# Performance work log

Measured on AMD Instinct MI355X. Metric: run time of the kernel, lower is better.

## Reference

```python
import math
import jax, jax.numpy as jnp
import numpy as np

B, N, D = 4, 4096, 1024
H, M = 16, 64
HD = D // H  # 64
EPS = 1e-6


def favor_features(data, proj):
    # data: [B,H,N,hd], proj: [M,hd] -> [B,H,N,M]
    hd = data.shape[-1]
    m = proj.shape[0]
    dn = data / math.sqrt(hd)
    norm_sq = 0.5 * jnp.sum(dn * dn, axis=-1, keepdims=True)  # [B,H,N,1]
    comb = jnp.einsum('bhnd,md->bhnm', dn, proj) - norm_sq
    comb = comb - jnp.max(comb, axis=-1, keepdims=True)
    return jnp.exp(comb) / math.sqrt(m) + EPS


def setup_inputs() -> dict:
    key = jax.random.key(0)
    ks = jax.random.split(key, 6)
    x = jax.random.normal(ks[0], (B, N, D), dtype=jnp.float32)
    qkv_w = jax.random.normal(ks[1], (3 * D, D), dtype=jnp.float32) * (1.0 / math.sqrt(D))
    qkv_b = jnp.zeros((3 * D,), dtype=jnp.float32)
    proj_w = jax.random.normal(ks[2], (D, D), dtype=jnp.float32) * (1.0 / math.sqrt(D))
    proj_b = jnp.zeros((D,), dtype=jnp.float32)
    pm = jax.random.normal(ks[3], (M, HD), dtype=jnp.float32)
    pm = pm / jnp.linalg.norm(pm, axis=-1, keepdims=True)
    return {"x": x, "qkv_w": qkv_w, "qkv_b": qkv_b, "proj_w": proj_w,
            "proj_b": proj_b, "projection_matrix": pm}


def reference(x, qkv_w, qkv_b, proj_w, proj_b, projection_matrix):
    b, n, d = x.shape
    qkv = x @ qkv_w.T + qkv_b                      # [B,N,3D]
    qkv = qkv.reshape(b, n, 3, H, HD)
    qkv = jnp.transpose(qkv, (2, 0, 3, 1, 4))      # [3,B,H,N,hd]
    q, k, v = qkv[0], qkv[1], qkv[2]
    q_p = favor_features(q, projection_matrix)     # [B,H,N,M]
    k_p = favor_features(k, projection_matrix)     # [B,H,N,M]
    kv = jnp.einsum('bhnm,bhnv->bhmv', k_p, v)     # [B,H,M,hd]
    out = jnp.einsum('bhnm,bhmv->bhnv', q_p, kv)   # [B,H,N,hd]
    k_sum = jnp.sum(k_p, axis=2)                   # [B,H,M]
    normalizer = jnp.einsum('bhnm,bhm->bhn', q_p, k_sum)[..., None]
    out = out / (normalizer + EPS)
    out = jnp.transpose(out, (0, 2, 1, 3)).reshape(b, n, d)
    return out @ proj_w.T + proj_b
```

## Files before the change

### kernel.cpp

```cpp
#include <hip/hip_runtime.h>
#include <math.h>

#define B_  4
#define N_  4096
#define D_  1024
#define H_  16
#define HD_ 64
#define M_  64
#define TD_ 3072
#define EPS_ 1e-6f

typedef __attribute__((ext_vector_type(8))) short short8;
typedef __attribute__((ext_vector_type(4))) float floatx4;
typedef unsigned int uint32;
typedef unsigned short ushort;

__device__ __forceinline__ void cvt2(float f0, float f1, uint32& hp, uint32& lp)
{
    uint32 b0 = __float_as_uint(f0), b1 = __float_as_uint(f1);
    hp = (b1 & 0xFFFF0000u) | (b0 >> 16);
    float l0 = f0 - __uint_as_float(b0 & 0xFFFF0000u);
    float l1 = f1 - __uint_as_float(b1 & 0xFFFF0000u);
    lp = (__float_as_uint(l1) & 0xFFFF0000u) | (__float_as_uint(l0) >> 16);
}

__global__ __launch_bounds__(256) void split_kernel(
    const float* __restrict__ src, ushort* __restrict__ hi,
    ushort* __restrict__ lo, int n)
{
    size_t i = ((size_t)blockIdx.x * 256 + threadIdx.x) * 8;
    if (i >= (size_t)n) return;
    float4 f0 = *(const float4*)(src + i);
    float4 f1 = *(const float4*)(src + i + 4);
    uint4 h, l;
    cvt2(f0.x, f0.y, h.x, l.x); cvt2(f0.z, f0.w, h.y, l.y);
    cvt2(f1.x, f1.y, h.z, l.z); cvt2(f1.z, f1.w, h.w, l.w);
    *(uint4*)(hi + i) = h;
    *(uint4*)(lo + i) = l;
}

#define LDSTR 40

__global__ __launch_bounds__(256, 2) void gemm_presplit_nt_bias(
    const ushort* __restrict__ Ah, const ushort* __restrict__ Al,
    const ushort* __restrict__ Bh, const ushort* __restrict__ Bl,
    const float* __restrict__ bias, float* __restrict__ C,
    int Nx, int Kx)
{
    __shared__ __align__(16) ushort AhiS[128*LDSTR], AloS[128*LDSTR];
    __shared__ __align__(16) ushort BhiS[128*LDSTR], BloS[128*LDSTR];

    const int t    = threadIdx.x;
    const int bm   = blockIdx.y * 128, bn = blockIdx.x * 128;
    const int lane = t & 63, wave = t >> 6;
    const int wm   = wave >> 1, wn = wave & 1;
    const int l16  = lane & 15, quad = lane >> 4;
    const int r    = t >> 1;
    const int ko   = (t & 1) * 16;

    floatx4 acc[4][4];
#pragma unroll
    for (int i = 0; i < 4; i++)
#pragma unroll
        for (int j = 0; j < 4; j++) acc[i][j] = (floatx4)0.f;

    const ushort* aph = Ah + (size_t)(bm + r) * Kx + ko;
    const ushort* apl = Al + (size_t)(bm + r) * Kx + ko;
    const ushort* bph = Bh + (size_t)(bn + r) * Kx + ko;
    const ushort* bpl = Bl + (size_t)(bn + r) * Kx + ko;

    for (int k0 = 0; k0 < Kx; k0 += 32) {
        uint4 vah0 = *(const uint4*)(aph + k0);
        uint4 vah1 = *(const uint4*)(aph + k0 + 8);
        uint4 val0 = *(const uint4*)(apl + k0);
        uint4 val1 = *(const uint4*)(apl + k0 + 8);
        uint4 vbh0 = *(const uint4*)(bph + k0);
        uint4 vbh1 = *(const uint4*)(bph + k0 + 8);
        uint4 vbl0 = *(const uint4*)(bpl + k0);
        uint4 vbl1 = *(const uint4*)(bpl + k0 + 8);

        __syncthreads();

        *(uint4*)&AhiS[r*LDSTR + ko]     = vah0;
        *(uint4*)&AhiS[r*LDSTR + ko + 8] = vah1;
        *(uint4*)&AloS[r*LDSTR + ko]     = val0;
        *(uint4*)&AloS[r*LDSTR + ko + 8] = val1;
        *(uint4*)&BhiS[r*LDSTR + ko]     = vbh0;
        *(uint4*)&BhiS[r*LDSTR + ko + 8] = vbh1;
        *(uint4*)&BloS[r*LDSTR + ko]     = vbl0;
        *(uint4*)&BloS[r*LDSTR + ko + 8] = vbl1;

        __syncthreads();

        short8 ah[4], al[4], bh[4], bl[4];
#pragma unroll
        for (int mi = 0; mi < 4; mi++) {
            int row = (wm*64 + mi*16 + l16) * LDSTR + quad*8;
            ah[mi] = *(const short8*)&AhiS[row];
            al[mi] = *(const short8*)&AloS[row];
        }
#pragma unroll
        for (int ni = 0; ni < 4; ni++) {
            int row = (wn*64 + ni*16 + l16) * LDSTR + quad*8;
            bh[ni] = *(const short8*)&BhiS[row];
            bl[ni] = *(const short8*)&BloS[row];
        }
#pragma unroll
        for (int mi = 0; mi < 4; mi++)
#pragma unroll
            for (int ni = 0; ni < 4; ni++) {
                floatx4 d = acc[mi][ni];
                d = __builtin_amdgcn_mfma_f32_16x16x32_bf16(ah[mi], bh[ni], d, 0, 0, 0);
                d = __builtin_amdgcn_mfma_f32_16x16x32_bf16(al[mi], bh[ni], d, 0, 0, 0);
                d = __builtin_amdgcn_mfma_f32_16x16x32_bf16(ah[mi], bl[ni], d, 0, 0, 0);
                acc[mi][ni] = d;
            }
    }

    float bia[4];
#pragma unroll
    for (int ni = 0; ni < 4; ni++)
        bia[ni] = bias[bn + wn*64 + ni*16 + l16];
#pragma unroll
    for (int mi = 0; mi < 4; mi++)
#pragma unroll
        for (int rr = 0; rr < 4; rr++) {
            int row = bm + wm*64 + mi*16 + quad*4 + rr;
            float* crow = C + (size_t)row * Nx + bn + wn*64 + l16;
#pragma unroll
            for (int ni = 0; ni < 4; ni++)
                crow[ni*16] = acc[mi][ni][rr] + bia[ni];
        }
}

__device__ __forceinline__ void gload16(const void* g, void* l)
{
    __builtin_amdgcn_global_load_lds(
        (const __attribute__((address_space(1))) unsigned int*)g,
        (__attribute__((address_space(3))) unsigned int*)l,
        16, 0, 0);
}

#define BAR()  asm volatile("s_barrier" ::: "memory")

__global__ __launch_bounds__(512, 2) void gemm256_pipe(
    const ushort* __restrict__ Ah, const ushort* __restrict__ Al,
    const ushort* __restrict__ Bh, const ushort* __restrict__ Bl,
    const float* __restrict__ bias, float* __restrict__ C,
    int Nx, int Kx)
{
    __shared__ __align__(16) ushort lds[65536];

    const int t    = threadIdx.x;
    const int wave = t >> 6, lane = t & 63;
    const int wm   = wave >> 2, wn = wave & 3;
    const int l16  = lane & 15, quad = lane >> 4;

    const int gx  = gridDim.x;
    const int nwg = gx * gridDim.y;
    int bid = blockIdx.y * gx + blockIdx.x;
    const int cpx = nwg >> 3;
    bid = (bid & 7) * cpx + (bid >> 3);
    const int bm = (bid / gx) * 256;
    const int bn = (bid % gx) * 256;

    const int r0   = t >> 2;
    const int cswz = ((((t & 3) << 4) ^ ((t & 0x18) << 1)) >> 1);
    const size_t aOff = (size_t)(bm + r0) * Kx + cswz;
    const size_t bOff = (size_t)(bn + r0) * Kx + cswz;

    const int ucol = (quad * 8) ^ ((l16 & 6) << 2);
    const int aRB  = (wm * 64 + l16) * 32 + ucol;
    const int bRB  = (wn * 32 + l16) * 32 + ucol;

    floatx4 acc[8][4];
#pragma unroll
    for (int i = 0; i < 8; i++)
#pragma unroll
        for (int j = 0; j < 4; j++) acc[i][j] = (floatx4)0.f;

#define STAGE_A2(NB, KT) do {                                                 \
    size_t g0_ = (size_t)(KT) * 32;                                           \
    gload16(Ah + aOff + g0_,                   &lds[(NB) + wave*512]);        \
    gload16(Al + aOff + g0_,                   &lds[(NB) + 8192 + wave*512]); \
    gload16(Ah + aOff + (size_t)128*Kx + g0_,  &lds[(NB) + 4096 + wave*512]); \
    gload16(Al + aOff + (size_t)128*Kx + g0_,  &lds[(NB) + 12288 + wave*512]);\
} while (0)
#define STAGE_B2(NB, KT) do {                                                 \
    size_t g0_ = (size_t)(KT) * 32;                                           \
    gload16(Bh + bOff + g0_,                   &lds[(NB) + 16384 + wave*512]);\
    gload16(Bl + bOff + g0_,                   &lds[(NB) + 24576 + wave*512]);\
    gload16(Bh + bOff + (size_t)128*Kx + g0_,  &lds[(NB) + 20480 + wave*512]);\
    gload16(Bl + bOff + (size_t)128*Kx + g0_,  &lds[(NB) + 28672 + wave*512]);\
} while (0)

    const int NT = Kx >> 5;

    STAGE_A2(0, 0);
    STAGE_B2(0, 0);
    asm volatile("s_waitcnt vmcnt(0)" ::: "memory");
    BAR();

    for (int kt = 0; kt < NT; kt++) {
        const int cb  = (kt & 1) << 15;
        const int nb  = cb ^ 32768;
        const int ktn = (kt + 1 < NT) ? kt + 1 : NT - 1;

        short8 ah_[4], al_[4], bh_[4], bl_[4];
        const int aB0 = cb + aRB;
        const int bB0 = cb + 16384 + bRB;

        STAGE_A2(nb, ktn);
        STAGE_B2(nb, ktn);

#pragma unroll
        for (int g = 0; g < 4; g++) {
            bh_[g] = *(const short8*)&lds[bB0 + (g >> 1)*4096 + (g & 1)*512];
            bl_[g] = *(const short8*)&lds[bB0 + 8192 + (g >> 1)*4096 + (g & 1)*512];
        }
#pragma unroll
        for (int mi = 0; mi < 4; mi++) {
            ah_[mi] = *(const short8*)&lds[aB0 + mi*512];
            al_[mi] = *(const short8*)&lds[aB0 + 8192 + mi*512];
        }
        __builtin_amdgcn_s_setprio(1);
#pragma unroll
        for (int mi = 0; mi < 4; mi++)
#pragma unroll
            for (int g = 0; g < 4; g++) {
                floatx4 d = acc[mi][g];
                d = __builtin_amdgcn_mfma_f32_16x16x32_bf16(ah_[mi], bh_[g], d, 0, 0, 0);
                d = __builtin_amdgcn_mfma_f32_16x16x32_bf16(al_[mi], bh_[g], d, 0, 0, 0);
                d = __builtin_amdgcn_mfma_f32_16x16x32_bf16(ah_[mi], bl_[g], d, 0, 0, 0);
                acc[mi][g] = d;
            }
        __builtin_amdgcn_s_setprio(0);

#pragma unroll
        for (int mi = 0; mi < 4; mi++) {
            ah_[mi] = *(const short8*)&lds[aB0 + 4096 + mi*512];
            al_[mi] = *(const short8*)&lds[aB0 + 12288 + mi*512];
        }
        __builtin_amdgcn_s_setprio(1);
#pragma unroll
        for (int mi = 0; mi < 4; mi++)
#pragma unroll
            for (int g = 0; g < 4; g++) {
                floatx4 d = acc[4 + mi][g];
                d = __builtin_amdgcn_mfma_f32_16x16x32_bf16(ah_[mi], bh_[g], d, 0, 0, 0);
                d = __builtin_amdgcn_mfma_f32_16x16x32_bf16(al_[mi], bh_[g], d, 0, 0, 0);
                d = __builtin_amdgcn_mfma_f32_16x16x32_bf16(ah_[mi], bl_[g], d, 0, 0, 0);
                acc[4 + mi][g] = d;
            }
        __builtin_amdgcn_s_setprio(0);

        asm volatile("s_waitcnt vmcnt(0)" ::: "memory");
        BAR();
    }

#pragma unroll
    for (int f = 0; f < 8; f++) {
        const int row = bm + (f >> 2)*128 + wm*64 + (f & 3)*16 + quad*4;
#pragma unroll
        for (int g = 0; g < 4; g++) {
            const int col = bn + (g >> 1)*128 + wn*32 + (g & 1)*16 + l16;
            const float bb = bias[col];
#pragma unroll
            for (int rr = 0; rr < 4; rr++)
                C[(size_t)(row + rr) * Nx + col] = acc[f][g][rr] + bb;
        }
    }
#undef STAGE_A2
#undef STAGE_B2
}

__global__ __launch_bounds__(256) void favor_features_kernel(
    const float* __restrict__ qkvb, const float* __restrict__ proj,
    float* __restrict__ qp, float* __restrict__ kp)
{
    __shared__ float  projT[64*64];
    __shared__ float4 dnbuf[4][64];
    const int t = threadIdx.x;
    const int wave = t >> 6, lane = t & 63;
    const int part = blockIdx.y;
    float* outp = (part == 0) ? qp : kp;

    for (int i = t; i < 4096; i += 256)
        projT[(i & 63) * 64 + (i >> 6)] = proj[i];
    __syncthreads();

    const int h = blockIdx.x >> 6;
    const int n0 = (blockIdx.x & 63) * 64;
    const float* src = qkvb + part * D_ + h * HD_ + lane;

    for (int iter = 0; iter < 4; iter++) {
        const int n = n0 + iter * 16 + wave * 4;
        float v0 = src[(size_t)(n+0) * TD_];
        float v1 = src[(size_t)(n+1) * TD_];
        float v2 = src[(size_t)(n+2) * TD_];
        float v3 = src[(size_t)(n+3) * TD_];
        float4 dn = make_float4(v0*0.125f, v1*0.125f, v2*0.125f, v3*0.125f);
        dnbuf[wave][lane] = dn;
        float s0 = dn.x*dn.x, s1 = dn.y*dn.y, s2 = dn.z*dn.z, s3 = dn.w*dn.w;
#pragma unroll
        for (int off = 32; off >= 1; off >>= 1) {
            s0 += __shfl_xor(s0, off, 64);
            s1 += __shfl_xor(s1, off, 64);
            s2 += __shfl_xor(s2, off, 64);
            s3 += __shfl_xor(s3, off, 64);
        }
        float c0 = -0.5f*s0, c1 = -0.5f*s1, c2 = -0.5f*s2, c3 = -0.5f*s3;
#pragma unroll
        for (int d = 0; d < 64; d++) {
            float p = projT[d*64 + lane];
            float4 q = dnbuf[wave][d];
            c0 = fmaf(q.x, p, c0);
            c1 = fmaf(q.y, p, c1);
            c2 = fmaf(q.z, p, c2);
            c3 = fmaf(q.w, p, c3);
        }
        float m0 = c0, m1 = c1, m2 = c2, m3 = c3;
#pragma unroll
        for (int off = 32; off >= 1; off >>= 1) {
            m0 = fmaxf(m0, __shfl_xor(m0, off, 64));
            m1 = fmaxf(m1, __shfl_xor(m1, off, 64));
            m2 = fmaxf(m2, __shfl_xor(m2, off, 64));
            m3 = fmaxf(m3, __shfl_xor(m3, off, 64));
        }
        float r0 = expf(c0 - m0) * 0.125f + EPS_;
        float r1 = expf(c1 - m1) * 0.125f + EPS_;
        float r2 = expf(c2 - m2) * 0.125f + EPS_;
        float r3 = expf(c3 - m3) * 0.125f + EPS_;
        size_t orow = ((size_t)h * N_ + n) * 64 + lane;
        outp[orow]       = r0;
        outp[orow + 64]  = r1;
        outp[orow + 128] = r2;
        outp[orow + 192] = r3;
    }
}

__global__ __launch_bounds__(256) void kv_partial_kernel(
    const float* __restrict__ qkvb, const float* __restrict__ kp,
    float* __restrict__ kvpart, float* __restrict__ kspart)
{
    const int t = threadIdx.x;
    const int h = blockIdx.x;
    const int c = blockIdx.y;
    const int n0 = c * 128;
    const int m0 = (t & 15) * 4;
    const int v0 = (t >> 4) * 4;

    const float* kpsrc = kp + ((size_t)h * N_ + n0) * 64 + m0;
    const float* vsrc  = qkvb + (size_t)n0 * TD_ + 2 * D_ + h * HD_ + v0;

    float acc[4][4];
#pragma unroll
    for (int i = 0; i < 4; i++)
#pragma unroll
        for (int j = 0; j < 4; j++) acc[i][j] = 0.f;
    float ks[4] = {0.f, 0.f, 0.f, 0.f};

#pragma unroll 4
    for (int n = 0; n < 128; n++) {
        float4 kq = *(const float4*)(kpsrc + (size_t)n * 64);
        float4 vq = *(const float4*)(vsrc  + (size_t)n * TD_);
        acc[0][0] = fmaf(kq.x, vq.x, acc[0][0]);
        acc[0][1] = fmaf(kq.x, vq.y, acc[0][1]);
        acc[0][2] = fmaf(kq.x, vq.z, acc[0][2]);
        acc[0][3] = fmaf(kq.x, vq.w, acc[0][3]);
        acc[1][0] = fmaf(kq.y, vq.x, acc[1][0]);
        acc[1][1] = fmaf(kq.y, vq.y, acc[1][1]);
        acc[1][2] = fmaf(kq.y, vq.z, acc[1][2]);
        acc[1][3] = fmaf(kq.y, vq.w, acc[1][3]);
        acc[2][0] = fmaf(kq.z, vq.x, acc[2][0]);
        acc[2][1] = fmaf(kq.z, vq.y, acc[2][1]);
        acc[2][2] = fmaf(kq.z, vq.z, acc[2][2]);
        acc[2][3] = fmaf(kq.z, vq.w, acc[2][3]);
        acc[3][0] = fmaf(kq.w, vq.x, acc[3][0]);
        acc[3][1] = fmaf(kq.w, vq.y, acc[3][1]);
        acc[3][2] = fmaf(kq.w, vq.z, acc[3][2]);
        acc[3][3] = fmaf(kq.w, vq.w, acc[3][3]);
        if (v0 == 0) {
            ks[0] += kq.x; ks[1] += kq.y; ks[2] += kq.z; ks[3] += kq.w;
        }
    }

    float* kvp = kvpart + (((size_t)h * 32 + c) * 4096) + m0 * 64 + v0;
#pragma unroll
    for (int i = 0; i < 4; i++)
        *(float4*)(kvp + i * 64) = make_float4(acc[i][0], acc[i][1], acc[i][2], acc[i][3]);

    if (v0 == 0) {
        float* ksp = kspart + ((size_t)h * 32 + c) * 64 + m0;
        *(float4*)ksp = make_float4(ks[0], ks[1], ks[2], ks[3]);
    }
}

__global__ __launch_bounds__(256) void kv_reduce_kernel(
    const float* __restrict__ kvpart, const float* __restrict__ kspart,
    float* __restrict__ kv, float* __restrict__ ksum)
{
    const int t = threadIdx.x;
    const int h = blockIdx.x;
    const int e0 = (blockIdx.y * 256 + t) * 4;

    float4 s = make_float4(0.f, 0.f, 0.f, 0.f);
    float kss = 0.f;
    const bool doks = (blockIdx.y == 0) && (t < 64);

    for (int c = 0; c < 32; c++) {
        float4 x = *(const float4*)(kvpart + (((size_t)h * 32 + c) * 4096) + e0);
        s.x += x.x; s.y += x.y; s.z += x.z; s.w += x.w;
        if (doks) kss += kspart[((size_t)h * 32 + c) * 64 + t];
    }

    *(float4*)(kv + (size_t)h * 4096 + e0) = s;
    if (doks) ksum[h * 64 + t] = kss;
}

__global__ __launch_bounds__(256) void out_kernel(
    const float* __restrict__ qp, const float* __restrict__ kv,
    const float* __restrict__ ksum, ushort* __restrict__ attn_hi,
    ushort* __restrict__ attn_lo)
{
    __shared__ float  kvs[4096];
    __shared__ float  kss[64];
    __shared__ float4 qbuf[4][64];
    const int t = threadIdx.x, lane = t & 63, wave = t >> 6;
    const int h = blockIdx.x;
    const int n0 = blockIdx.y * 64;

    for (int i = t; i < 4096; i += 256) kvs[i] = kv[(size_t)h * 4096 + i];
    if (t < 64) kss[t] = ksum[h * 64 + t];
    __syncthreads();

    const float* qsrc = qp + (size_t)h * N_ * 64 + lane;
    const size_t dbase = h * HD_ + lane;

    for (int iter = 0; iter < 4; iter++) {
        const int n = n0 + iter * 16 + wave * 4;
        float q0 = qsrc[(size_t)(n+0) * 64];
        float q1 = qsrc[(size_t)(n+1) * 64];
        float q2 = qsrc[(size_t)(n+2) * 64];
        float q3 = qsrc[(size_t)(n+3) * 64];
        qbuf[wave][lane] = make_float4(q0, q1, q2, q3);
        float t0 = q0 * kss[lane], t1 = q1 * kss[lane];
        float t2 = q2 * kss[lane], t3 = q3 * kss[lane];
#pragma unroll
        for (int off = 32; off >= 1; off >>= 1) {
            t0 += __shfl_xor(t0, off, 64);
            t1 += __shfl_xor(t1, off, 64);
            t2 += __shfl_xor(t2, off, 64);
            t3 += __shfl_xor(t3, off, 64);
        }
        float a0 = 0.f, a1 = 0.f, a2 = 0.f, a3 = 0.f;
#pragma unroll
        for (int m = 0; m < 64; m++) {
            float kvv = kvs[m*64 + lane];
            float4 q = qbuf[wave][m];
            a0 = fmaf(q.x, kvv, a0);
            a1 = fmaf(q.y, kvv, a1);
            a2 = fmaf(q.z, kvv, a2);
            a3 = fmaf(q.w, kvv, a3);
        }
        float r[4];
        r[0] = a0 / (t0 + EPS_); r[1] = a1 / (t1 + EPS_);
        r[2] = a2 / (t2 + EPS_); r[3] = a3 / (t3 + EPS_);
#pragma unroll
        for (int i = 0; i < 4; i++) {
            uint32 bits = __float_as_uint(r[i]);
            float lof = r[i] - __uint_as_float(bits & 0xFFFF0000u);
            size_t idx = (size_t)(n + i) * D_ + dbase;
            attn_hi[idx] = (ushort)(bits >> 16);
            attn_lo[idx] = (ushort)(__float_as_uint(lof) >> 16);
        }
    }
}

extern "C" void kernel_launch(void* const* d_in, const int* in_sizes, int n_in,
                              void* d_out, int out_size, void* d_ws, size_t ws_size,
                              hipStream_t stream)
{
    const float* x      = (const float*)d_in[0];
    const float* qkv_w  = (const float*)d_in[1];
    const float* qkv_b  = (const float*)d_in[2];
    const float* proj_w = (const float*)d_in[3];
    const float* proj_b = (const float*)d_in[4];
    const float* pm     = (const float*)d_in[5];
    float* out = (float*)d_out;
    float* ws  = (float*)d_ws;

    const bool tierA = ws_size >= 327553024ULL;
    const bool tierB = ws_size >= 176558080ULL;

    if (tierA) {
        float* qkvbA  = ws;
        float* qp     = qkvbA + 50331648;
        float* kp     = qp + 4194304;
        float* kvb    = kp + 4194304;
        float* ksum   = kvb + 65536;
        float* kvpart = ksum + 1024;
        float* kspart = kvpart + 2097152;
        float* axw    = kspart + 32768;
        float* wsplit = axw + 16777216;

        ushort* xw_hi    = (ushort*)axw;
        ushort* xw_lo    = xw_hi + 16777216;
        ushort* attn_hi  = xw_hi;
        ushort* attn_lo  = xw_lo;
        ushort* qkvw_hi  = (ushort*)wsplit;
        ushort* qkvw_lo  = qkvw_hi + 3145728;
        ushort* projw_hi = qkvw_lo + 3145728;
        ushort* projw_lo = projw_hi + 1048576;

        split_kernel<<<1536, 256, 0, stream>>>(qkv_w, qkvw_hi, qkvw_lo, TD_*D_);
        split_kernel<<<512,  256, 0, stream>>>(proj_w, projw_hi, projw_lo, D_*D_);
        split_kernel<<<8192, 256, 0, stream>>>(x, xw_hi, xw_lo, B_*N_*D_);

        gemm256_pipe<<<dim3(12, 64), 512, 0, stream>>>(
            xw_hi, xw_lo, qkvw_hi, qkvw_lo, qkv_b, qkvbA, TD_, D_);

        for (int b = 0; b < B_; b++) {
            const float* qkvb = qkvbA + (size_t)b * N_ * TD_;
            dim3 g2(1024, 2);
            favor_features_kernel<<<g2, 256, 0, stream>>>(qkvb, pm, qp, kp);
            dim3 g3(16, 32);
            kv_partial_kernel<<<g3, 256, 0, stream>>>(qkvb, kp, kvpart, kspart);
            kv_reduce_kernel<<<dim3(16, 4), 256, 0, stream>>>(kvpart, kspart, kvb, ksum);
            dim3 g4(16, 64);
            out_kernel<<<g4, 256, 0, stream>>>(qp, kvb, ksum,
                attn_hi + (size_t)b * N_ * D_, attn_lo + (size_t)b * N_ * D_);
        }

        gemm256_pipe<<<dim3(4, 64), 512, 0, stream>>>(
            attn_hi, attn_lo, projw_hi, projw_lo, proj_b, out, D_, D_);
    } else if (tierB) {
        float* qkvb   = ws;
        float* qp     = ws + 12582912;
        float* kp     = qp + 4194304;
        float* kvb    = kp + 4194304;
        float* ksum   = kvb + 65536;
        float* kvpart = ksum + 1024;
        float* kspart = kvpart + 2097152;
        float* wsplit = kspart + 32768;
        float* attnA  = wsplit + 4194304;

        ushort* xw_hi    = (ushort*)qp;
        ushort* xw_lo    = xw_hi + 4194304;
        ushort* qkvw_hi  = (ushort*)wsplit;
        ushort* qkvw_lo  = qkvw_hi + 3145728;
        ushort* projw_hi = qkvw_lo + 3145728;
        ushort* projw_lo = projw_hi + 1048576;
        ushort* attnA_hi = (ushort*)attnA;
        ushort* attnA_lo = attnA_hi + 16777216;

        split_kernel<<<1536, 256, 0, stream>>>(qkv_w, qkvw_hi, qkvw_lo, TD_*D_);
        split_kernel<<<512,  256, 0, stream>>>(proj_w, projw_hi, projw_lo, D_*D_);

        for (int b = 0; b < B_; b++) {
            const float* xb = x + (size_t)b * N_ * D_;
            split_kernel<<<2048, 256, 0, stream>>>(xb, xw_hi, xw_lo, N_*D_);
            gemm256_pipe<<<dim3(12, 16), 512, 0, stream>>>(
                xw_hi, xw_lo, qkvw_hi, qkvw_lo, qkv_b, qkvb, TD_, D_);
            dim3 g2(1024, 2);
            favor_features_kernel<<<g2, 256, 0, stream>>>(qkvb, pm, qp, kp);
            dim3 g3(16, 32);
            kv_partial_kernel<<<g3, 256, 0, stream>>>(qkvb, kp, kvpart, kspart);
            kv_reduce_kernel<<<dim3(16, 4), 256, 0, stream>>>(kvpart, kspart, kvb, ksum);
            dim3 g4(16, 64);
            out_kernel<<<g4, 256, 0, stream>>>(qp, kvb, ksum,
                attnA_hi + (size_t)b * N_ * D_, attnA_lo + (size_t)b * N_ * D_);
        }

        gemm256_pipe<<<dim3(4, 64), 512, 0, stream>>>(
            attnA_hi, attnA_lo, projw_hi, projw_lo, proj_b, out, D_, D_);
    } else {
        float* qkvb   = ws;
        float* qpreg  = ws + 12582912;
        float* kpreg  = qpreg + 4194304;
        float* kvb    = kpreg + 4194304;
        float* ksum   = kvb + 65536;
        float* kvpart = ksum + 1024;
        float* kspart = kvpart + 2097152;
        float* wsplit = kspart + 32768;

        ushort* xw_hi   = (ushort*)qpreg;
        ushort* xw_lo   = xw_hi + 4194304;
        float*  qp      = qpreg;
        float*  kp      = kpreg;
        ushort* attn_hi = (ushort*)kpreg;
        ushort* attn_lo = attn_hi + 4194304;
        ushort* qkvw_hi = (ushort*)wsplit;
        ushort* qkvw_lo = qkvw_hi + 3145728;
        ushort* projw_hi= qkvw_lo + 3145728;
        ushort* projw_lo= projw_hi + 1048576;

        split_kernel<<<TD_*D_/2048, 256, 0, stream>>>(qkv_w, qkvw_hi, qkvw_lo, TD_*D_);
        split_kernel<<<D_*D_/2048,  256, 0, stream>>>(proj_w, projw_hi, projw_lo, D_*D_);

        for (int b = 0; b < B_; b++) {
            const float* xb = x + (size_t)b * N_ * D_;
            float* outb = out + (size_t)b * N_ * D_;

            split_kernel<<<N_*D_/2048, 256, 0, stream>>>(xb, xw_hi, xw_lo, N_*D_);

            gemm256_pipe<<<dim3(12, 16), 512, 0, stream>>>(
                xw_hi, xw_lo, qkvw_hi, qkvw_lo, qkv_b, qkvb, TD_, D_);

            dim3 g2(1024, 2);
            favor_features_kernel<<<g2, 256, 0, stream>>>(qkvb, pm, qp, kp);

            dim3 g3(16, 32);
            kv_partial_kernel<<<g3, 256, 0, stream>>>(qkvb, kp, kvpart, kspart);
            kv_reduce_kernel<<<dim3(16, 4), 256, 0, stream>>>(kvpart, kspart, kvb, ksum);

            dim3 g4(16, 64);
            out_kernel<<<g4, 256, 0, stream>>>(qp, kvb, ksum, attn_hi, attn_lo);

            dim3 g5(D_ / 128, N_ / 128);
            gemm_presplit_nt_bias<<<g5, 256, 0, stream>>>(
                attn_hi, attn_lo, projw_hi, projw_lo, proj_b, outb, D_, D_);
        }
    }
}
```

Before: 949.1 us.

## Fuse FAVOR feature map with KV accumulation via atomics and reschedule GEMM staging

Merges the q/k feature-map kernel, the KV partial kernel and the KV reduce kernel into one kernel. K features are kept in shared memory instead of being written to global, and per-chunk partials are reduced with float atomicAdd into a buffer zeroed by a new small kernel. Separately, the pipelined GEMM now issues the B-tile staging after the first MFMA half, with explicit lgkmcnt waits and scheduling barriers, to spread global loads across the compute. Atomics make the KV summation order nondeterministic, and the fused kernel uses more LDS per block.

```diff
diff --git a/kernel.cpp b/kernel.cpp
--- a/kernel.cpp
+++ b/kernel.cpp
@@ -39,6 +39,12 @@
     *(uint4*)(lo + i) = l;
 }
 
+__global__ __launch_bounds__(256) void zero_kernel(float* __restrict__ p)
+{
+    int i = (blockIdx.x * 256 + threadIdx.x) * 4;
+    if (i < 66560) *(float4*)(p + i) = make_float4(0.f, 0.f, 0.f, 0.f);
+}
+
 #define LDSTR 40
 
 __global__ __launch_bounds__(256, 2) void gemm_presplit_nt_bias(
@@ -142,6 +148,7 @@
 }
 
 #define BAR()  asm volatile("s_barrier" ::: "memory")
+#define SBAR() __builtin_amdgcn_sched_barrier(0)
 
 __global__ __launch_bounds__(512, 2) void gemm256_pipe(
     const ushort* __restrict__ Ah, const ushort* __restrict__ Al,
@@ -211,7 +218,6 @@
         const int bB0 = cb + 16384 + bRB;
 
         STAGE_A2(nb, ktn);
-        STAGE_B2(nb, ktn);
 
 #pragma unroll
         for (int g = 0; g < 4; g++) {
@@ -223,6 +229,8 @@
             ah_[mi] = *(const short8*)&lds[aB0 + mi*512];
             al_[mi] = *(const short8*)&lds[aB0 + 8192 + mi*512];
         }
+        asm volatile("s_waitcnt lgkmcnt(0)" ::: "memory");
+        SBAR();
         __builtin_amdgcn_s_setprio(1);
 #pragma unroll
         for (int mi = 0; mi < 4; mi++)
@@ -235,12 +243,16 @@
                 acc[mi][g] = d;
             }
         __builtin_amdgcn_s_setprio(0);
-
+        SBAR();
+
+        STAGE_B2(nb, ktn);
 #pragma unroll
         for (int mi = 0; mi < 4; mi++) {
             ah_[mi] = *(const short8*)&lds[aB0 + 4096 + mi*512];
             al_[mi] = *(const short8*)&lds[aB0 + 12288 + mi*512];
         }
+        asm volatile("s_waitcnt lgkmcnt(0)" ::: "memory");
+        SBAR();
         __builtin_amdgcn_s_setprio(1);
 #pragma unroll
         for (int mi = 0; mi < 4; mi++)
@@ -253,6 +265,7 @@
                 acc[4 + mi][g] = d;
             }
         __builtin_amdgcn_s_setprio(0);
+        SBAR();
 
         asm volatile("s_waitcnt vmcnt(0)" ::: "memory");
         BAR();
@@ -274,84 +287,87 @@
 #undef STAGE_B2
 }
 
-__global__ __launch_bounds__(256) void favor_features_kernel(
+__global__ __launch_bounds__(256) void favor_kv_kernel(
     const float* __restrict__ qkvb, const float* __restrict__ proj,
-    float* __restrict__ qp, float* __restrict__ kp)
+    float* __restrict__ qp, float* __restrict__ kvb, float* __restrict__ ksum)
 {
     __shared__ float  projT[64*64];
+    __shared__ float  kpL[128*64];
     __shared__ float4 dnbuf[4][64];
-    const int t = threadIdx.x;
-    const int wave = t >> 6, lane = t & 63;
-    const int part = blockIdx.y;
-    float* outp = (part == 0) ? qp : kp;
+    const int t = threadIdx.x, wave = t >> 6, lane = t & 63;
+    const int h  = blockIdx.x;
+    const int n0 = blockIdx.y * 128;
 
     for (int i = t; i < 4096; i += 256)
         projT[(i & 63) * 64 + (i >> 6)] = proj[i];
     __syncthreads();
 
-    const int h = blockIdx.x >> 6;
-    const int n0 = (blockIdx.x & 63) * 64;
-    const float* src = qkvb + part * D_ + h * HD_ + lane;
-
-    for (int iter = 0; iter < 4; iter++) {
-        const int n = n0 + iter * 16 + wave * 4;
-        float v0 = src[(size_t)(n+0) * TD_];
-        float v1 = src[(size_t)(n+1) * TD_];
-        float v2 = src[(size_t)(n+2) * TD_];
-        float v3 = src[(size_t)(n+3) * TD_];
-        float4 dn = make_float4(v0*0.125f, v1*0.125f, v2*0.125f, v3*0.125f);
-        dnbuf[wave][lane] = dn;
-        float s0 = dn.x*dn.x, s1 = dn.y*dn.y, s2 = dn.z*dn.z, s3 = dn.w*dn.w;
-#pragma unroll
-        for (int off = 32; off >= 1; off >>= 1) {
-            s0 += __shfl_xor(s0, off, 64);
-            s1 += __shfl_xor(s1, off, 64);
-            s2 += __shfl_xor(s2, off, 64);
-            s3 += __shfl_xor(s3, off, 64);
-        }
-        float c0 = -0.5f*s0, c1 = -0.5f*s1, c2 = -0.5f*s2, c3 = -0.5f*s3;
-#pragma unroll
-        for (int d = 0; d < 64; d++) {
-            float p = projT[d*64 + lane];
-            float4 q = dnbuf[wave][d];
-            c0 = fmaf(q.x, p, c0);
-            c1 = fmaf(q.y, p, c1);
-            c2 = fmaf(q.z, p, c2);
-            c3 = fmaf(q.w, p, c3);
-        }
-        float m0 = c0, m1 = c1, m2 = c2, m3 = c3;
-#pragma unroll
-        for (int off = 32; off >= 1; off >>= 1) {
-            m0 = fmaxf(m0, __shfl_xor(m0, off, 64));
-            m1 = fmaxf(m1, __shfl_xor(m1, off, 64));
-            m2 = fmaxf(m2, __shfl_xor(m2, off, 64));
-            m3 = fmaxf(m3, __shfl_xor(m3, off, 64));
-        }
-        float r0 = expf(c0 - m0) * 0.125f + EPS_;
-        float r1 = expf(c1 - m1) * 0.125f + EPS_;
-        float r2 = expf(c2 - m2) * 0.125f + EPS_;
-        float r3 = expf(c3 - m3) * 0.125f + EPS_;
+#define FAVOR_ROWS(PART, EMIT)                                                \
+    {                                                                         \
+        const float* src = qkvb + (PART) * D_ + h * HD_ + lane;               \
+        for (int iter = 0; iter < 8; iter++) {                                \
+            const int n = n0 + iter * 16 + wave * 4;                          \
+            float v0 = src[(size_t)(n+0) * TD_];                              \
+            float v1 = src[(size_t)(n+1) * TD_];                              \
+            float v2 = src[(size_t)(n+2) * TD_];                              \
+            float v3 = src[(size_t)(n+3) * TD_];                              \
+            float4 dn = make_float4(v0*0.125f, v1*0.125f, v2*0.125f, v3*0.125f); \
+            dnbuf[wave][lane] = dn;                                           \
+            float s0 = dn.x*dn.x, s1 = dn.y*dn.y, s2 = dn.z*dn.z, s3 = dn.w*dn.w; \
+            _Pragma("unroll")                                                 \
+            for (int off = 32; off >= 1; off >>= 1) {                         \
+                s0 += __shfl_xor(s0, off, 64);                                \
+                s1 += __shfl_xor(s1, off, 64);                                \
+                s2 += __shfl_xor(s2, off, 64);                                \
+                s3 += __shfl_xor(s3, off, 64);                                \
+            }                                                                 \
+            float c0 = -0.5f*s0, c1 = -0.5f*s1, c2 = -0.5f*s2, c3 = -0.5f*s3; \
+            _Pragma("unroll")                                                 \
+            for (int d = 0; d < 64; d++) {                                    \
+                float p = projT[d*64 + lane];                                 \
+                float4 q = dnbuf[wave][d];                                    \
+                c0 = fmaf(q.x, p, c0);                                        \
+                c1 = fmaf(q.y, p, c1);                                        \
+                c2 = fmaf(q.z, p, c2);                                        \
+                c3 = fmaf(q.w, p, c3);                                        \
+            }                                                                 \
+            float m0 = c0, m1 = c1, m2 = c2, m3 = c3;                         \
+            _Pragma("unroll")                                                 \
+            for (int off = 32; off >= 1; off >>= 1) {                         \
+                m0 = fmaxf(m0, __shfl_xor(m0, off, 64));                      \
+                m1 = fmaxf(m1, __shfl_xor(m1, off, 64));                      \
+                m2 = fmaxf(m2, __shfl_xor(m2, off, 64));                      \
+                m3 = fmaxf(m3, __shfl_xor(m3, off, 64));                      \
+            }                                                                 \
+            float r0 = expf(c0 - m0) * 0.125f + EPS_;                         \
+            float r1 = expf(c1 - m1) * 0.125f + EPS_;                         \
+            float r2 = expf(c2 - m2) * 0.125f + EPS_;                         \
+            float r3 = expf(c3 - m3) * 0.125f + EPS_;                         \
+            EMIT;                                                             \
+        }                                                                     \
+    }
+
+    FAVOR_ROWS(0, {
         size_t orow = ((size_t)h * N_ + n) * 64 + lane;
-        outp[orow]       = r0;
-        outp[orow + 64]  = r1;
-        outp[orow + 128] = r2;
-        outp[orow + 192] = r3;
-    }
-}
-
-__global__ __launch_bounds__(256) void kv_partial_kernel(
-    const float* __restrict__ qkvb, const float* __restrict__ kp,
-    float* __restrict__ kvpart, float* __restrict__ kspart)
-{
-    const int t = threadIdx.x;
-    const int h = blockIdx.x;
-    const int c = blockIdx.y;
-    const int n0 = c * 128;
+        qp[orow]       = r0;
+        qp[orow + 64]  = r1;
+        qp[orow + 128] = r2;
+        qp[orow + 192] = r3;
+    });
+
+    FAVOR_ROWS(1, {
+        int lr = (n - n0) * 64 + lane;
+        kpL[lr]       = r0;
+        kpL[lr + 64]  = r1;
+        kpL[lr + 128] = r2;
+        kpL[lr + 192] = r3;
+    });
+#undef FAVOR_ROWS
+    __syncthreads();
+
     const int m0 = (t & 15) * 4;
     const int v0 = (t >> 4) * 4;
-
-    const float* kpsrc = kp + ((size_t)h * N_ + n0) * 64 + m0;
-    const float* vsrc  = qkvb + (size_t)n0 * TD_ + 2 * D_ + h * HD_ + v0;
+    const float* vsrc = qkvb + (size_t)n0 * TD_ + 2 * D_ + h * HD_ + v0;
 
     float acc[4][4];
 #pragma unroll
@@ -362,8 +378,8 @@
 
 #pragma unroll 4
     for (int n = 0; n < 128; n++) {
-        float4 kq = *(const float4*)(kpsrc + (size_t)n * 64);
-        float4 vq = *(const float4*)(vsrc  + (size_t)n * TD_);
+        float4 kq = *(const float4*)&kpL[n * 64 + m0];
+        float4 vq = *(const float4*)(vsrc + (size_t)n * TD_);
         acc[0][0] = fmaf(kq.x, vq.x, acc[0][0]);
         acc[0][1] = fmaf(kq.x, vq.y, acc[0][1]);
         acc[0][2] = fmaf(kq.x, vq.z, acc[0][2]);
@@ -385,37 +401,18 @@
         }
     }
 
-    float* kvp = kvpart + (((size_t)h * 32 + c) * 4096) + m0 * 64 + v0;
+    float* kvp = kvb + (size_t)h * 4096 + m0 * 64 + v0;
 #pragma unroll
     for (int i = 0; i < 4; i++)
-        *(float4*)(kvp + i * 64) = make_float4(acc[i][0], acc[i][1], acc[i][2], acc[i][3]);
+#pragma unroll
+        for (int j = 0; j < 4; j++)
+            atomicAdd(kvp + i * 64 + j, acc[i][j]);
 
     if (v0 == 0) {
-        float* ksp = kspart + ((size_t)h * 32 + c) * 64 + m0;
-        *(float4*)ksp = make_float4(ks[0], ks[1], ks[2], ks[3]);
-    }
-}
-
-__global__ __launch_bounds__(256) void kv_reduce_kernel(
-    const float* __restrict__ kvpart, const float* __restrict__ kspart,
-    float* __restrict__ kv, float* __restrict__ ksum)
-{
-    const int t = threadIdx.x;
-    const int h = blockIdx.x;
-    const int e0 = (blockIdx.y * 256 + t) * 4;
-
-    float4 s = make_float4(0.f, 0.f, 0.f, 0.f);
-    float kss = 0.f;
-    const bool doks = (blockIdx.y == 0) && (t < 64);
-
-    for (int c = 0; c < 32; c++) {
-        float4 x = *(const float4*)(kvpart + (((size_t)h * 32 + c) * 4096) + e0);
-        s.x += x.x; s.y += x.y; s.z += x.z; s.w += x.w;
-        if (doks) kss += kspart[((size_t)h * 32 + c) * 64 + t];
-    }
-
-    *(float4*)(kv + (size_t)h * 4096 + e0) = s;
-    if (doks) ksum[h * 64 + t] = kss;
+#pragma unroll
+        for (int i = 0; i < 4; i++)
+            atomicAdd(ksum + h * 64 + m0 + i, ks[i]);
+    }
 }
 
 __global__ __launch_bounds__(256) void out_kernel(
@@ -522,13 +519,10 @@
 
         for (int b = 0; b < B_; b++) {
             const float* qkvb = qkvbA + (size_t)b * N_ * TD_;
-            dim3 g2(1024, 2);
-            favor_features_kernel<<<g2, 256, 0, stream>>>(qkvb, pm, qp, kp);
-            dim3 g3(16, 32);
-            kv_partial_kernel<<<g3, 256, 0, stream>>>(qkvb, kp, kvpart, kspart);
-            kv_reduce_kernel<<<dim3(16, 4), 256, 0, stream>>>(kvpart, kspart, kvb, ksum);
-            dim3 g4(16, 64);
-            out_kernel<<<g4, 256, 0, stream>>>(qp, kvb, ksum,
+            zero_kernel<<<65, 256, 0, stream>>>(kvb);
+            favor_kv_kernel<<<dim3(16, 32), 256, 0, stream>>>(
+                qkvb, pm, qp, kvb, ksum);
+            out_kernel<<<dim3(16, 64), 256, 0, stream>>>(qp, kvb, ksum,
                 attn_hi + (size_t)b * N_ * D_, attn_lo + (size_t)b * N_ * D_);
         }
 
@@ -562,13 +556,10 @@
             split_kernel<<<2048, 256, 0, stream>>>(xb, xw_hi, xw_lo, N_*D_);
             gemm256_pipe<<<dim3(12, 16), 512, 0, stream>>>(
                 xw_hi, xw_lo, qkvw_hi, qkvw_lo, qkv_b, qkvb, TD_, D_);
-            dim3 g2(1024, 2);
-            favor_features_kernel<<<g2, 256, 0, stream>>>(qkvb, pm, qp, kp);
-            dim3 g3(16, 32);
-            kv_partial_kernel<<<g3, 256, 0, stream>>>(qkvb, kp, kvpart, kspart);
-            kv_reduce_kernel<<<dim3(16, 4), 256, 0, stream>>>(kvpart, kspart, kvb, ksum);
-            dim3 g4(16, 64);
-            out_kernel<<<g4, 256, 0, stream>>>(qp, kvb, ksum,
+            zero_kernel<<<65, 256, 0, stream>>>(kvb);
+            favor_kv_kernel<<<dim3(16, 32), 256, 0, stream>>>(
+                qkvb, pm, qp, kvb, ksum);
+            out_kernel<<<dim3(16, 64), 256, 0, stream>>>(qp, kvb, ksum,
                 attnA_hi + (size_t)b * N_ * D_, attnA_lo + (size_t)b * N_ * D_);
         }
 
@@ -587,7 +578,6 @@
         ushort* xw_hi   = (ushort*)qpreg;
         ushort* xw_lo   = xw_hi + 4194304;
         float*  qp      = qpreg;
-        float*  kp      = kpreg;
         ushort* attn_hi = (ushort*)kpreg;
         ushort* attn_lo = attn_hi + 4194304;
         ushort* qkvw_hi = (ushort*)wsplit;
@@ -607,15 +597,11 @@
             gemm256_pipe<<<dim3(12, 16), 512, 0, stream>>>(
                 xw_hi, xw_lo, qkvw_hi, qkvw_lo, qkv_b, qkvb, TD_, D_);
 
-            dim3 g2(1024, 2);
-            favor_features_kernel<<<g2, 256, 0, stream>>>(qkvb, pm, qp, kp);
-
-            dim3 g3(16, 32);
-            kv_partial_kernel<<<g3, 256, 0, stream>>>(qkvb, kp, kvpart, kspart);
-            kv_reduce_kernel<<<dim3(16, 4), 256, 0, stream>>>(kvpart, kspart, kvb, ksum);
-
-            dim3 g4(16, 64);
-            out_kernel<<<g4, 256, 0, stream>>>(qp, kvb, ksum, attn_hi, attn_lo);
+            zero_kernel<<<65, 256, 0, stream>>>(kvb);
+            favor_kv_kernel<<<dim3(16, 32), 256, 0, stream>>>(
+                qkvb, pm, qp, kvb, ksum);
+
+            out_kernel<<<dim3(16, 64), 256, 0, stream>>>(qp, kvb, ksum, attn_hi, attn_lo);
 
             dim3 g5(D_ / 128, N_ / 128);
             gemm_presplit_nt_bias<<<g5, 256, 0, stream>>>(
```

After: 1.009 ms. +6.4%, slower.

## Replace KV partial+reduce with atomic accumulation and reschedule GEMM B staging

Applied to the files above, without the earlier changes.

The separate KV partial-write and reduce kernels are replaced by a single kernel that atomically adds per-chunk KV and k-sum contributions into a buffer zeroed by a new tiny kernel. This removes the partial buffers and one launch per batch, at the cost of float atomics with nondeterministic summation order. In the pipelined GEMM, the B-tile global-to-LDS staging moves between the two MFMA halves, with explicit lgkmcnt waits and scheduling barriers added to control instruction ordering. Workspace tier thresholds shrink to match the removed buffers.

```diff
diff --git a/kernel.cpp b/kernel.cpp
--- a/kernel.cpp
+++ b/kernel.cpp
@@ -39,6 +39,12 @@
     *(uint4*)(lo + i) = l;
 }
 
+__global__ __launch_bounds__(256) void zero_kernel(float* __restrict__ p)
+{
+    int i = (blockIdx.x * 256 + threadIdx.x) * 4;
+    if (i < 66560) *(float4*)(p + i) = make_float4(0.f, 0.f, 0.f, 0.f);
+}
+
 #define LDSTR 40
 
 __global__ __launch_bounds__(256, 2) void gemm_presplit_nt_bias(
@@ -142,6 +148,7 @@
 }
 
 #define BAR()  asm volatile("s_barrier" ::: "memory")
+#define SBAR() __builtin_amdgcn_sched_barrier(0)
 
 __global__ __launch_bounds__(512, 2) void gemm256_pipe(
     const ushort* __restrict__ Ah, const ushort* __restrict__ Al,
@@ -211,7 +218,6 @@
         const int bB0 = cb + 16384 + bRB;
 
         STAGE_A2(nb, ktn);
-        STAGE_B2(nb, ktn);
 
 #pragma unroll
         for (int g = 0; g < 4; g++) {
@@ -223,6 +229,8 @@
             ah_[mi] = *(const short8*)&lds[aB0 + mi*512];
             al_[mi] = *(const short8*)&lds[aB0 + 8192 + mi*512];
         }
+        asm volatile("s_waitcnt lgkmcnt(0)" ::: "memory");
+        SBAR();
         __builtin_amdgcn_s_setprio(1);
 #pragma unroll
         for (int mi = 0; mi < 4; mi++)
@@ -235,12 +243,16 @@
                 acc[mi][g] = d;
             }
         __builtin_amdgcn_s_setprio(0);
-
+        SBAR();
+
+        STAGE_B2(nb, ktn);
 #pragma unroll
         for (int mi = 0; mi < 4; mi++) {
             ah_[mi] = *(const short8*)&lds[aB0 + 4096 + mi*512];
             al_[mi] = *(const short8*)&lds[aB0 + 12288 + mi*512];
         }
+        asm volatile("s_waitcnt lgkmcnt(0)" ::: "memory");
+        SBAR();
         __builtin_amdgcn_s_setprio(1);
 #pragma unroll
         for (int mi = 0; mi < 4; mi++)
@@ -253,6 +265,7 @@
                 acc[4 + mi][g] = d;
             }
         __builtin_amdgcn_s_setprio(0);
+        SBAR();
 
         asm volatile("s_waitcnt vmcnt(0)" ::: "memory");
         BAR();
@@ -339,9 +352,9 @@
     }
 }
 
-__global__ __launch_bounds__(256) void kv_partial_kernel(
+__global__ __launch_bounds__(256) void kv_partial_atomic(
     const float* __restrict__ qkvb, const float* __restrict__ kp,
-    float* __restrict__ kvpart, float* __restrict__ kspart)
+    float* __restrict__ kvb, float* __restrict__ ksum)
 {
     const int t = threadIdx.x;
     const int h = blockIdx.x;
@@ -385,37 +398,18 @@
         }
     }
 
-    float* kvp = kvpart + (((size_t)h * 32 + c) * 4096) + m0 * 64 + v0;
+    float* kvp = kvb + (size_t)h * 4096 + m0 * 64 + v0;
 #pragma unroll
     for (int i = 0; i < 4; i++)
-        *(float4*)(kvp + i * 64) = make_float4(acc[i][0], acc[i][1], acc[i][2], acc[i][3]);
+#pragma unroll
+        for (int j = 0; j < 4; j++)
+            atomicAdd(kvp + i * 64 + j, acc[i][j]);
 
     if (v0 == 0) {
-        float* ksp = kspart + ((size_t)h * 32 + c) * 64 + m0;
-        *(float4*)ksp = make_float4(ks[0], ks[1], ks[2], ks[3]);
-    }
-}
-
-__global__ __launch_bounds__(256) void kv_reduce_kernel(
-    const float* __restrict__ kvpart, const float* __restrict__ kspart,
-    float* __restrict__ kv, float* __restrict__ ksum)
-{
-    const int t = threadIdx.x;
-    const int h = blockIdx.x;
-    const int e0 = (blockIdx.y * 256 + t) * 4;
-
-    float4 s = make_float4(0.f, 0.f, 0.f, 0.f);
-    float kss = 0.f;
-    const bool doks = (blockIdx.y == 0) && (t < 64);
-
-    for (int c = 0; c < 32; c++) {
-        float4 x = *(const float4*)(kvpart + (((size_t)h * 32 + c) * 4096) + e0);
-        s.x += x.x; s.y += x.y; s.z += x.z; s.w += x.w;
-        if (doks) kss += kspart[((size_t)h * 32 + c) * 64 + t];
-    }
-
-    *(float4*)(kv + (size_t)h * 4096 + e0) = s;
-    if (doks) ksum[h * 64 + t] = kss;
+#pragma unroll
+        for (int i = 0; i < 4; i++)
+            atomicAdd(ksum + h * 64 + m0 + i, ks[i]);
+    }
 }
 
 __global__ __launch_bounds__(256) void out_kernel(
@@ -490,8 +484,8 @@
     float* out = (float*)d_out;
     float* ws  = (float*)d_ws;
 
-    const bool tierA = ws_size >= 327553024ULL;
-    const bool tierB = ws_size >= 176558080ULL;
+    const bool tierA = ws_size >= 319033344ULL;
+    const bool tierB = ws_size >= 168038400ULL;
 
     if (tierA) {
         float* qkvbA  = ws;
@@ -499,9 +493,7 @@
         float* kp     = qp + 4194304;
         float* kvb    = kp + 4194304;
         float* ksum   = kvb + 65536;
-        float* kvpart = ksum + 1024;
-        float* kspart = kvpart + 2097152;
-        float* axw    = kspart + 32768;
+        float* axw    = ksum + 1024;
         float* wsplit = axw + 16777216;
 
         ushort* xw_hi    = (ushort*)axw;
@@ -522,13 +514,10 @@
 
         for (int b = 0; b < B_; b++) {
             const float* qkvb = qkvbA + (size_t)b * N_ * TD_;
-            dim3 g2(1024, 2);
-            favor_features_kernel<<<g2, 256, 0, stream>>>(qkvb, pm, qp, kp);
-            dim3 g3(16, 32);
-            kv_partial_kernel<<<g3, 256, 0, stream>>>(qkvb, kp, kvpart, kspart);
-            kv_reduce_kernel<<<dim3(16, 4), 256, 0, stream>>>(kvpart, kspart, kvb, ksum);
-            dim3 g4(16, 64);
-            out_kernel<<<g4, 256, 0, stream>>>(qp, kvb, ksum,
+            zero_kernel<<<65, 256, 0, stream>>>(kvb);
+            favor_features_kernel<<<dim3(1024, 2), 256, 0, stream>>>(qkvb, pm, qp, kp);
+            kv_partial_atomic<<<dim3(16, 32), 256, 0, stream>>>(qkvb, kp, kvb, ksum);
+            out_kernel<<<dim3(16, 64), 256, 0, stream>>>(qp, kvb, ksum,
                 attn_hi + (size_t)b * N_ * D_, attn_lo + (size_t)b * N_ * D_);
         }
 
@@ -540,9 +529,7 @@
         float* kp     = qp + 4194304;
         float* kvb    = kp + 4194304;
         float* ksum   = kvb + 65536;
-        float* kvpart = ksum + 1024;
-        float* kspart = kvpart + 2097152;
-        float* wsplit = kspart + 32768;
+        float* wsplit = ksum + 1024;
         float* attnA  = wsplit + 4194304;
 
         ushort* xw_hi    = (ushort*)qp;
@@ -562,13 +549,10 @@
             split_kernel<<<2048, 256, 0, stream>>>(xb, xw_hi, xw_lo, N_*D_);
             gemm256_pipe<<<dim3(12, 16), 512, 0, stream>>>(
                 xw_hi, xw_lo, qkvw_hi, qkvw_lo, qkv_b, qkvb, TD_, D_);
-            dim3 g2(1024, 2);
-            favor_features_kernel<<<g2, 256, 0, stream>>>(qkvb, pm, qp, kp);
-            dim3 g3(16, 32);
-            kv_partial_kernel<<<g3, 256, 0, stream>>>(qkvb, kp, kvpart, kspart);
-            kv_reduce_kernel<<<dim3(16, 4), 256, 0, stream>>>(kvpart, kspart, kvb, ksum);
-            dim3 g4(16, 64);
-            out_kernel<<<g4, 256, 0, stream>>>(qp, kvb, ksum,
+            zero_kernel<<<65, 256, 0, stream>>>(kvb);
+            favor_features_kernel<<<dim3(1024, 2), 256, 0, stream>>>(qkvb, pm, qp, kp);
+            kv_partial_atomic<<<dim3(16, 32), 256, 0, stream>>>(qkvb, kp, kvb, ksum);
+            out_kernel<<<dim3(16, 64), 256, 0, stream>>>(qp, kvb, ksum,
                 attnA_hi + (size_t)b * N_ * D_, attnA_lo + (size_t)b * N_ * D_);
         }
 
@@ -580,9 +564,7 @@
         float* kpreg  = qpreg + 4194304;
         float* kvb    = kpreg + 4194304;
         float* ksum   = kvb + 65536;
-        float* kvpart = ksum + 1024;
-        float* kspart = kvpart + 2097152;
-        float* wsplit = kspart + 32768;
+        float* wsplit = ksum + 1024;
 
         ushort* xw_hi   = (ushort*)qpreg;
         ushort* xw_lo   = xw_hi + 4194304;
@@ -607,15 +589,11 @@
             gemm256_pipe<<<dim3(12, 16), 512, 0, stream>>>(
                 xw_hi, xw_lo, qkvw_hi, qkvw_lo, qkv_b, qkvb, TD_, D_);
 
-            dim3 g2(1024, 2);
-            favor_features_kernel<<<g2, 256, 0, stream>>>(qkvb, pm, qp, kp);
-
-            dim3 g3(16, 32);
-            kv_partial_kernel<<<g3, 256, 0, stream>>>(qkvb, kp, kvpart, kspart);
-            kv_reduce_kernel<<<dim3(16, 4), 256, 0, stream>>>(kvpart, kspart, kvb, ksum);
-
-            dim3 g4(16, 64);
-            out_kernel<<<g4, 256, 0, stream>>>(qp, kvb, ksum, attn_hi, attn_lo);
+            zero_kernel<<<65, 256, 0, stream>>>(kvb);
+            favor_features_kernel<<<dim3(1024, 2), 256, 0, stream>>>(qkvb, pm, qp, kp);
+            kv_partial_atomic<<<dim3(16, 32), 256, 0, stream>>>(qkvb, kp, kvb, ksum);
+
+            out_kernel<<<dim3(16, 64), 256, 0, stream>>>(qp, kvb, ksum, attn_hi, attn_lo);
 
             dim3 g5(D_ / 128, N_ / 128);
             gemm_presplit_nt_bias<<<g5, 256, 0, stream>>>(
```

Result: slower. 1.005 ms (+5.9%).
